# Kernel tuning notes

Hardware: AMD Instinct MI355X
Metric: run time of the kernel (lower is better)

Reference implementation:

```python
import math
import jax, jax.numpy as jnp
import numpy as np

INPUT_DIM = 512
HIDDEN_DIM = 512
BATCH = 8
SEQ_LEN = 4096


def _xavier(key, shape):
    fan_out, fan_in = shape
    limit = math.sqrt(6.0 / (fan_in + fan_out))
    return jax.random.uniform(key, shape, jnp.float32, -limit, limit)


def setup_inputs() -> dict:
    key = jax.random.key(0)
    kx, kA, kB, kC, kD, kWg = jax.random.split(key, 6)
    return {
        "x": jax.random.normal(kx, (BATCH, SEQ_LEN, INPUT_DIM), jnp.float32),
        "A": jax.random.uniform(kA, (HIDDEN_DIM,), jnp.float32, 0.8, 0.95),
        "B": _xavier(kB, (HIDDEN_DIM, INPUT_DIM)),
        "C": _xavier(kC, (HIDDEN_DIM, HIDDEN_DIM)),
        "D": _xavier(kD, (HIDDEN_DIM, INPUT_DIM)),
        "Wg": _xavier(kWg, (HIDDEN_DIM, INPUT_DIM)),
        "bias_h": jnp.zeros((HIDDEN_DIM,), jnp.float32),
        "bias_y": jnp.zeros((HIDDEN_DIM,), jnp.float32),
    }


def reference(x, A, B, C, D, Wg, bias_h, bias_y):
    # x: (b, t, i). Eval mode: dropout is identity.
    hidden_dim = A.shape[0]
    # Precompute all input-dependent per-step terms as batched GEMMs.
    g = jnp.clip(jax.nn.sigmoid(jnp.einsum('bti,hi->bth', x, Wg)), 0.05, 0.95)
    xB = jnp.einsum('bti,hi->bth', x, B)
    # h_t = h_{t-1} + g_t*(A*h_{t-1} + xB_t + bias_h - h_{t-1})
    #     = (1 - g_t*(1 - A)) * h_{t-1} + g_t*(xB_t + bias_h)
    a_coef = 1.0 - g * (1.0 - A)          # (b, t, h)
    b_coef = g * (xB + bias_h)            # (b, t, h)

    def step(h, ab):
        a_t, b_t = ab
        h = a_t * h + b_t
        return h, h

    h0 = jnp.zeros((x.shape[0], hidden_dim), x.dtype)
    _, hs = jax.lax.scan(step, h0, (jnp.swapaxes(a_coef, 0, 1), jnp.swapaxes(b_coef, 0, 1)))
    hs = jnp.swapaxes(hs, 0, 1)           # (b, t, h)

    scale = 1.0 / math.sqrt(hidden_dim)
    y = (jnp.einsum('bth,oh->bto', hs, C) + jnp.einsum('bti,hi->bth', x, D) + bias_y) * scale
    return y
```

## Files before the change

### kernel.cpp

```cpp
#include <hip/hip_runtime.h>
#include <math.h>

#define MTOT 32768
#define KD 512
#define HD 512
#define NB 8
#define TS 4096
#define NCHUNK 64
#define TCHUNK 64

typedef __attribute__((ext_vector_type(8))) short bf16x8;
typedef __attribute__((ext_vector_type(4))) float f32x4;
typedef __attribute__((ext_vector_type(4))) unsigned short us4;

#define GLD16(gsrc, ldst) __builtin_amdgcn_global_load_lds( \
    (const __attribute__((address_space(1))) void*)(gsrc),   \
    (__attribute__((address_space(3))) void*)(ldst), 16, 0, 0)

__device__ __forceinline__ unsigned short f2bf(float f) {
    unsigned u = __float_as_uint(f);
    return (unsigned short)((u + 0x7FFFu + ((u >> 16) & 1u)) >> 16);
}
__device__ __forceinline__ float bf2f(unsigned short u) {
    return __uint_as_float(((unsigned)u) << 16);
}

__global__ __launch_bounds__(256) void cast_all(
    const float* __restrict__ x, const float* __restrict__ B,
    const float* __restrict__ G, const float* __restrict__ C,
    const float* __restrict__ D,
    unsigned short* __restrict__ x16, unsigned short* __restrict__ w16)
{
    const int blk = blockIdx.x;
    const float* src;
    unsigned short* dst;
    int i;
    if (blk < (MTOT * KD / 1024)) {
        src = x; dst = x16;
        i = blk * 1024 + threadIdx.x * 4;
    } else {
        const int r = blk - (MTOT * KD / 1024);
        const int mat = r >> 8;
        src = (mat == 0) ? B : (mat == 1) ? G : (mat == 2) ? C : D;
        dst = w16 + (size_t)mat * (HD * KD);
        i = (r & 255) * 1024 + threadIdx.x * 4;
    }
    float4 v = *(const float4*)(src + i);
    us4 o; o.x = f2bf(v.x); o.y = f2bf(v.y); o.z = f2bf(v.z); o.w = f2bf(v.w);
    *(us4*)(dst + i) = o;
}

__global__ __launch_bounds__(256, 3) void in_gemm_mfma(
    const short* __restrict__ xb, const short* __restrict__ wmat,
    const float* __restrict__ Avec, const float* __restrict__ bias_h,
    unsigned* __restrict__ ab16, float2* __restrict__ chPS)
{
    __shared__ __align__(16) short Xs[128 * 64];
    __shared__ __align__(16) short Ws[2][64 * 64];
    const int tid = threadIdx.x;
    const int w = tid >> 6, l = tid & 63;
    const int m0 = blockIdx.x * 128;
    const int n0 = blockIdx.y * 64;
    const int wm = (w & 1) * 64;
    const int wn = (w >> 1) * 32;

    int xsrc[4], xdst[4];
    #pragma unroll
    for (int j = 0; j < 4; ++j) {
        const int s = (w * 4 + j) * 64 + l;
        const int r = s >> 3, g = (s & 7) ^ (r & 7);
        xsrc[j] = (m0 + r) * KD + g * 8;
        xdst[j] = (w * 4 + j) * 64 * 8;
    }
    int wsrc[2], wdst[2];
    #pragma unroll
    for (int j = 0; j < 2; ++j) {
        const int s = (w * 2 + j) * 64 + l;
        const int r = s >> 3, g = (s & 7) ^ (r & 7);
        wsrc[j] = (n0 + r) * KD + g * 8;
        wdst[j] = (w * 2 + j) * 64 * 8;
    }

    f32x4 acc[2][4][2];
    #pragma unroll
    for (int a = 0; a < 2; ++a)
        #pragma unroll
        for (int i = 0; i < 4; ++i)
            #pragma unroll
            for (int j = 0; j < 2; ++j) acc[a][i][j] = (f32x4)0.0f;

    for (int kk = 0; kk < KD; kk += 64) {
        __syncthreads();
        #pragma unroll
        for (int j = 0; j < 4; ++j) GLD16(xb + xsrc[j] + kk, Xs + xdst[j]);
        #pragma unroll
        for (int mat = 0; mat < 2; ++mat)
            #pragma unroll
            for (int j = 0; j < 2; ++j)
                GLD16(wmat + (size_t)mat * (HD * KD) + wsrc[j] + kk, &Ws[mat][wdst[j]]);
        __syncthreads();
        #pragma unroll
        for (int kc = 0; kc < 2; ++kc) {
            const int g = kc * 4 + (l >> 4);
            bf16x8 af[4];
            #pragma unroll
            for (int mt = 0; mt < 4; ++mt) {
                const int r = wm + mt * 16 + (l & 15);
                af[mt] = *(const bf16x8*)(Xs + r * 64 + ((g ^ (r & 7)) * 8));
            }
            #pragma unroll
            for (int mat = 0; mat < 2; ++mat) {
                #pragma unroll
                for (int nt = 0; nt < 2; ++nt) {
                    const int r = wn + nt * 16 + (l & 15);
                    bf16x8 bfv = *(const bf16x8*)(&Ws[mat][r * 64 + ((g ^ (r & 7)) * 8)]);
                    #pragma unroll
                    for (int mt = 0; mt < 4; ++mt)
                        acc[mat][mt][nt] = __builtin_amdgcn_mfma_f32_16x16x32_bf16(
                            af[mt], bfv, acc[mat][mt][nt], 0, 0, 0);
                }
            }
        }
    }

    const int q  = l >> 4;
    const int cl = l & 15;
    const int bidx   = m0 >> 12;
    const int c_in_b = ((m0 & (TS - 1)) >> 6) + (w & 1);
    #pragma unroll
    for (int nt = 0; nt < 2; ++nt) {
        const int n = n0 + wn + nt * 16 + cl;
        const float An1 = 1.0f - Avec[n];
        const float bh  = bias_h[n];
        float Pc = 1.0f, Sc = 0.0f;
        #pragma unroll
        for (int mt = 0; mt < 4; ++mt) {
            float Pl = 1.0f, Sl = 0.0f;
            #pragma unroll
            for (int r = 0; r < 4; ++r) {
                const float vB = acc[0][mt][nt][r];
                const float vG = acc[1][mt][nt][r];
                float g = __builtin_amdgcn_rcpf(1.0f + __expf(-vG));
                g = fminf(fmaxf(g, 0.05f), 0.95f);
                const unsigned short su = f2bf(g * An1);
                const unsigned short bu = f2bf(g * (vB + bh));
                const float a  = 1.0f - bf2f(su);
                const float bb = bf2f(bu);
                const int m = m0 + wm + mt * 16 + q * 4 + r;
                ab16[(size_t)m * HD + n] = (unsigned)su | ((unsigned)bu << 16);
                Sl = fmaf(a, Sl, bb);
                Pl *= a;
            }
            float Pm = 1.0f, Sm = 0.0f;
            #pragma unroll
            for (int k = 0; k < 4; ++k) {
                const float Pk = __shfl(Pl, cl + 16 * k, 64);
                const float Sk = __shfl(Sl, cl + 16 * k, 64);
                Sm = fmaf(Pk, Sm, Sk);
                Pm *= Pk;
            }
            Sc = fmaf(Pm, Sc, Sm);
            Pc *= Pm;
        }
        if (q == 0) {
            chPS[(size_t)c_in_b * (NB * HD) + bidx * HD + n] = make_float2(Pc, Sc);
        }
    }
}

__global__ __launch_bounds__(256) void scan_pass3(
    const unsigned* __restrict__ ab, const float2* __restrict__ chPS,
    unsigned short* __restrict__ hs_out)
{
    const int g = blockIdx.x * blockDim.x + threadIdx.x;
    const int h = g & (HD - 1);
    const int rest = g >> 9;
    const int b = rest & (NB - 1);
    const int c = rest >> 3;
    const float2* p = chPS + (size_t)b * HD + h;
    float hv = 0.0f;
    for (int j = 0; j < c; ++j) {
        const float2 ps = p[(size_t)j * (NB * HD)];
        hv = fmaf(ps.x, hv, ps.y);
    }
    size_t idx = ((size_t)(b * TS + c * TCHUNK)) * HD + h;
    #pragma unroll 4
    for (int t = 0; t < TCHUNK; ++t) {
        const unsigned v = ab[idx];
        const float a  = 1.0f - bf2f((unsigned short)(v & 0xFFFFu));
        const float bb = bf2f((unsigned short)(v >> 16));
        hv = fmaf(a, hv, bb);
        hs_out[idx] = f2bf(hv);
        idx += HD;
    }
}

__global__ __launch_bounds__(256, 2) void out_gemm_dual(
    const short* __restrict__ hs, const short* __restrict__ xb,
    const short* __restrict__ Cb, const short* __restrict__ Db,
    const float* __restrict__ bias_y, float* __restrict__ y)
{
    __shared__ __align__(16) short Hs[128 * 64];
    __shared__ __align__(16) short Xs2[128 * 64];
    __shared__ __align__(16) short Cs[128 * 64];
    __shared__ __align__(16) short Ds[128 * 64];
    const int tid = threadIdx.x;
    const int w = tid >> 6, l = tid & 63;
    const int m0 = blockIdx.x * 128;
    const int n0 = blockIdx.y * 128;
    const int wm = (w & 1) * 64;
    const int wn = (w >> 1) * 64;

    int src_m[4], src_n[4], dst_s[4];
    #pragma unroll
    for (int j = 0; j < 4; ++j) {
        const int s = (w * 4 + j) * 64 + l;
        const int r = s >> 3, g = (s & 7) ^ (r & 7);
        src_m[j] = (m0 + r) * HD + g * 8;
        src_n[j] = (n0 + r) * HD + g * 8;
        dst_s[j] = (w * 4 + j) * 64 * 8;
    }

    f32x4 acc[4][4];
    #pragma unroll
    for (int i = 0; i < 4; ++i)
        #pragma unroll
        for (int j = 0; j < 4; ++j) acc[i][j] = (f32x4)0.0f;

    for (int kk = 0; kk < HD; kk += 64) {
        __syncthreads();
        #pragma unroll
        for (int j = 0; j < 4; ++j) {
            GLD16(hs + src_m[j] + kk, Hs  + dst_s[j]);
            GLD16(xb + src_m[j] + kk, Xs2 + dst_s[j]);
            GLD16(Cb + src_n[j] + kk, Cs  + dst_s[j]);
            GLD16(Db + src_n[j] + kk, Ds  + dst_s[j]);
        }
        __syncthreads();
        #pragma unroll
        for (int kc = 0; kc < 2; ++kc) {
            const int g = kc * 4 + (l >> 4);
            {
                bf16x8 af[4], bfv[4];
                #pragma unroll
                for (int t = 0; t < 4; ++t) {
                    const int ra = wm + t * 16 + (l & 15);
                    af[t] = *(const bf16x8*)(Hs + ra * 64 + ((g ^ (ra & 7)) * 8));
                    const int rb = wn + t * 16 + (l & 15);
                    bfv[t] = *(const bf16x8*)(Cs + rb * 64 + ((g ^ (rb & 7)) * 8));
                }
                #pragma unroll
                for (int mt = 0; mt < 4; ++mt)
                    #pragma unroll
                    for (int nt = 0; nt < 4; ++nt)
                        acc[mt][nt] = __builtin_amdgcn_mfma_f32_16x16x32_bf16(
                            af[mt], bfv[nt], acc[mt][nt], 0, 0, 0);
            }
            {
                bf16x8 af[4], bfv[4];
                #pragma unroll
                for (int t = 0; t < 4; ++t) {
                    const int ra = wm + t * 16 + (l & 15);
                    af[t] = *(const bf16x8*)(Xs2 + ra * 64 + ((g ^ (ra & 7)) * 8));
                    const int rb = wn + t * 16 + (l & 15);
                    bfv[t] = *(const bf16x8*)(Ds + rb * 64 + ((g ^ (rb & 7)) * 8));
                }
                #pragma unroll
                for (int mt = 0; mt < 4; ++mt)
                    #pragma unroll
                    for (int nt = 0; nt < 4; ++nt)
                        acc[mt][nt] = __builtin_amdgcn_mfma_f32_16x16x32_bf16(
                            af[mt], bfv[nt], acc[mt][nt], 0, 0, 0);
            }
        }
    }

    const float scale = 0.04419417382415922f;
    #pragma unroll
    for (int nt = 0; nt < 4; ++nt) {
        const int n = n0 + wn + nt * 16 + (l & 15);
        const float by = bias_y[n];
        #pragma unroll
        for (int mt = 0; mt < 4; ++mt) {
            #pragma unroll
            for (int r = 0; r < 4; ++r) {
                const int m = m0 + wm + mt * 16 + (l >> 4) * 4 + r;
                y[(size_t)m * HD + n] = (acc[mt][nt][r] + by) * scale;
            }
        }
    }
}

extern "C" void kernel_launch(void* const* d_in, const int* in_sizes, int n_in,
                              void* d_out, int out_size, void* d_ws, size_t ws_size,
                              hipStream_t stream) {
    const float* x      = (const float*)d_in[0];
    const float* Avec   = (const float*)d_in[1];
    const float* Bw     = (const float*)d_in[2];
    const float* Cw     = (const float*)d_in[3];
    const float* Dw     = (const float*)d_in[4];
    const float* Wg     = (const float*)d_in[5];
    const float* bias_h = (const float*)d_in[6];
    const float* bias_y = (const float*)d_in[7];
    float* y = (float*)d_out;

    unsigned* ab16        = (unsigned*)d_ws;
    unsigned short* x16   = (unsigned short*)(ab16 + (size_t)MTOT * HD);
    unsigned short* hs16  = x16 + (size_t)MTOT * HD;
    unsigned short* w16   = hs16 + (size_t)MTOT * HD;
    float2* chPS = (float2*)(w16 + (size_t)4 * HD * KD);

    cast_all<<<MTOT * KD / 1024 + 4 * (HD * KD / 1024), 256, 0, stream>>>(
        x, Bw, Wg, Cw, Dw, x16, w16);

    in_gemm_mfma<<<dim3(MTOT / 128, HD / 64), 256, 0, stream>>>(
        (const short*)x16, (const short*)w16, Avec, bias_h, ab16, chPS);

    scan_pass3<<<(NB * HD * NCHUNK) / 256, 256, 0, stream>>>(ab16, chPS, hs16);

    out_gemm_dual<<<dim3(MTOT / 128, HD / 128), 256, 0, stream>>>(
        (const short*)hs16, (const short*)x16,
        (const short*)(w16 + (size_t)2 * HD * KD),
        (const short*)(w16 + (size_t)3 * HD * KD), bias_y, y);
}
```

Baseline: 248.9 us.

## Fuse chunked scan into input GEMM using decoupled lookback across blocks

Merges the scan pass into the input GEMM kernel. Blocks take a dynamic virtual id from an atomic counter, publish per-tile chunk aggregates with release flags, and walk back over predecessor aggregates to get the carry-in state. Each block then finishes the recurrence in registers and writes bf16 hidden states through an LDS transpose. This drops the packed a/b intermediate (a full global write and read) and one kernel launch. In exchange it adds a serial lookback that grows with position in the sequence, spin-waiting on other blocks, and a bounded guard that could produce wrong results if it ever times out.

```diff
diff --git a/kernel.cpp b/kernel.cpp
--- a/kernel.cpp
+++ b/kernel.cpp
@@ -6,8 +6,6 @@
 #define HD 512
 #define NB 8
 #define TS 4096
-#define NCHUNK 64
-#define TCHUNK 64
 
 typedef __attribute__((ext_vector_type(8))) short bf16x8;
 typedef __attribute__((ext_vector_type(4))) float f32x4;
@@ -29,9 +27,13 @@
     const float* __restrict__ x, const float* __restrict__ B,
     const float* __restrict__ G, const float* __restrict__ C,
     const float* __restrict__ D,
-    unsigned short* __restrict__ x16, unsigned short* __restrict__ w16)
+    unsigned short* __restrict__ x16, unsigned short* __restrict__ w16,
+    unsigned* __restrict__ flags)
 {
     const int blk = blockIdx.x;
+    if (blk == 0) {
+        for (int i = threadIdx.x; i < 2049; i += 256) flags[i] = 0u;
+    }
     const float* src;
     unsigned short* dst;
     int i;
@@ -50,17 +52,35 @@
     *(us4*)(dst + i) = o;
 }
 
-__global__ __launch_bounds__(256, 3) void in_gemm_mfma(
+__global__ __launch_bounds__(256, 3) void in_gemm_scan(
     const short* __restrict__ xb, const short* __restrict__ wmat,
     const float* __restrict__ Avec, const float* __restrict__ bias_h,
-    unsigned* __restrict__ ab16, float2* __restrict__ chPS)
+    unsigned short* __restrict__ hs_out,
+    unsigned long long* __restrict__ payload,
+    unsigned* __restrict__ flags)
 {
-    __shared__ __align__(16) short Xs[128 * 64];
-    __shared__ __align__(16) short Ws[2][64 * 64];
+    __shared__ __align__(16) char smem[(128 * 64 + 2 * 64 * 64) * 2];
+    short* Xs  = (short*)smem;
+    short* Ws0 = Xs + 128 * 64;
+    short* Ws1 = Ws0 + 64 * 64;
+    short* hsT = (short*)smem;
+    __shared__ float2 chunkAgg[2][64];
+    __shared__ float Eblk[64];
+    __shared__ unsigned vid_s;
+
     const int tid = threadIdx.x;
+    if (tid == 0) vid_s = atomicAdd(flags + 2048, 1u);
+    __syncthreads();
+    const unsigned vid = vid_s;
+    const int mxG = vid >> 3;
+    const int ny  = vid & 7;
+    const int m0 = mxG * 128;
+    const int n0 = ny * 64;
+    const int batch = mxG >> 5;
+    const int pos   = mxG & 31;
+    const int base_f = ny * 256 + batch * 32;
+
     const int w = tid >> 6, l = tid & 63;
-    const int m0 = blockIdx.x * 128;
-    const int n0 = blockIdx.y * 64;
     const int wm = (w & 1) * 64;
     const int wn = (w >> 1) * 32;
 
@@ -94,10 +114,10 @@
         #pragma unroll
         for (int j = 0; j < 4; ++j) GLD16(xb + xsrc[j] + kk, Xs + xdst[j]);
         #pragma unroll
-        for (int mat = 0; mat < 2; ++mat)
-            #pragma unroll
-            for (int j = 0; j < 2; ++j)
-                GLD16(wmat + (size_t)mat * (HD * KD) + wsrc[j] + kk, &Ws[mat][wdst[j]]);
+        for (int j = 0; j < 2; ++j) {
+            GLD16(wmat + wsrc[j] + kk, Ws0 + wdst[j]);
+            GLD16(wmat + (size_t)(HD * KD) + wsrc[j] + kk, Ws1 + wdst[j]);
+        }
         __syncthreads();
         #pragma unroll
         for (int kc = 0; kc < 2; ++kc) {
@@ -109,15 +129,17 @@
                 af[mt] = *(const bf16x8*)(Xs + r * 64 + ((g ^ (r & 7)) * 8));
             }
             #pragma unroll
-            for (int mat = 0; mat < 2; ++mat) {
-                #pragma unroll
-                for (int nt = 0; nt < 2; ++nt) {
-                    const int r = wn + nt * 16 + (l & 15);
-                    bf16x8 bfv = *(const bf16x8*)(&Ws[mat][r * 64 + ((g ^ (r & 7)) * 8)]);
-                    #pragma unroll
-                    for (int mt = 0; mt < 4; ++mt)
-                        acc[mat][mt][nt] = __builtin_amdgcn_mfma_f32_16x16x32_bf16(
-                            af[mt], bfv, acc[mat][mt][nt], 0, 0, 0);
+            for (int nt = 0; nt < 2; ++nt) {
+                const int r = wn + nt * 16 + (l & 15);
+                const int off = r * 64 + ((g ^ (r & 7)) * 8);
+                const bf16x8 bfB = *(const bf16x8*)(Ws0 + off);
+                const bf16x8 bfG = *(const bf16x8*)(Ws1 + off);
+                #pragma unroll
+                for (int mt = 0; mt < 4; ++mt) {
+                    acc[0][mt][nt] = __builtin_amdgcn_mfma_f32_16x16x32_bf16(
+                        af[mt], bfB, acc[0][mt][nt], 0, 0, 0);
+                    acc[1][mt][nt] = __builtin_amdgcn_mfma_f32_16x16x32_bf16(
+                        af[mt], bfG, acc[1][mt][nt], 0, 0, 0);
                 }
             }
         }
@@ -125,8 +147,7 @@
 
     const int q  = l >> 4;
     const int cl = l & 15;
-    const int bidx   = m0 >> 12;
-    const int c_in_b = ((m0 & (TS - 1)) >> 6) + (w & 1);
+    unsigned ab_pack[2][16];
     #pragma unroll
     for (int nt = 0; nt < 2; ++nt) {
         const int n = n0 + wn + nt * 16 + cl;
@@ -144,11 +165,9 @@
                 g = fminf(fmaxf(g, 0.05f), 0.95f);
                 const unsigned short su = f2bf(g * An1);
                 const unsigned short bu = f2bf(g * (vB + bh));
-                const float a  = 1.0f - bf2f(su);
-                const float bb = bf2f(bu);
-                const int m = m0 + wm + mt * 16 + q * 4 + r;
-                ab16[(size_t)m * HD + n] = (unsigned)su | ((unsigned)bu << 16);
-                Sl = fmaf(a, Sl, bb);
+                ab_pack[nt][mt * 4 + r] = (unsigned)su | ((unsigned)bu << 16);
+                const float a = 1.0f - bf2f(su);
+                Sl = fmaf(a, Sl, bf2f(bu));
                 Pl *= a;
             }
             float Pm = 1.0f, Sm = 0.0f;
@@ -162,36 +181,87 @@
             Sc = fmaf(Pm, Sc, Sm);
             Pc *= Pm;
         }
-        if (q == 0) {
-            chPS[(size_t)c_in_b * (NB * HD) + bidx * HD + n] = make_float2(Pc, Sc);
-        }
-    }
-}
-
-__global__ __launch_bounds__(256) void scan_pass3(
-    const unsigned* __restrict__ ab, const float2* __restrict__ chPS,
-    unsigned short* __restrict__ hs_out)
-{
-    const int g = blockIdx.x * blockDim.x + threadIdx.x;
-    const int h = g & (HD - 1);
-    const int rest = g >> 9;
-    const int b = rest & (NB - 1);
-    const int c = rest >> 3;
-    const float2* p = chPS + (size_t)b * HD + h;
-    float hv = 0.0f;
-    for (int j = 0; j < c; ++j) {
-        const float2 ps = p[(size_t)j * (NB * HD)];
-        hv = fmaf(ps.x, hv, ps.y);
-    }
-    size_t idx = ((size_t)(b * TS + c * TCHUNK)) * HD + h;
-    #pragma unroll 4
-    for (int t = 0; t < TCHUNK; ++t) {
-        const unsigned v = ab[idx];
-        const float a  = 1.0f - bf2f((unsigned short)(v & 0xFFFFu));
-        const float bb = bf2f((unsigned short)(v >> 16));
-        hv = fmaf(a, hv, bb);
-        hs_out[idx] = f2bf(hv);
-        idx += HD;
+        if (q == 0) chunkAgg[w & 1][wn + nt * 16 + cl] = make_float2(Pc, Sc);
+    }
+    __syncthreads();
+
+    if (tid < 64) {
+        const float2 c0 = chunkAgg[0][tid], c1 = chunkAgg[1][tid];
+        union { float2 f; unsigned long long u; } cv;
+        cv.f = make_float2(c1.x * c0.x, fmaf(c1.x, c0.y, c1.y));
+        __hip_atomic_store(&payload[(size_t)(base_f + pos) * 64 + tid], cv.u,
+                           __ATOMIC_RELAXED, __HIP_MEMORY_SCOPE_AGENT);
+    }
+    __syncthreads();
+    if (tid == 0)
+        __hip_atomic_store(&flags[base_f + pos], 1u,
+                           __ATOMIC_RELEASE, __HIP_MEMORY_SCOPE_AGENT);
+
+    if (tid < 64) {
+        float Pa = 1.0f, Sa = 0.0f;
+        for (int p = pos - 1; p >= 0; --p) {
+            int guard = 0;
+            while (__hip_atomic_load(&flags[base_f + p], __ATOMIC_ACQUIRE,
+                                     __HIP_MEMORY_SCOPE_AGENT) == 0u) {
+                __builtin_amdgcn_s_sleep(8);
+                if (++guard > (1 << 22)) break;
+            }
+            union { float2 f; unsigned long long u; } cv;
+            cv.u = __hip_atomic_load(&payload[(size_t)(base_f + p) * 64 + tid],
+                                     __ATOMIC_RELAXED, __HIP_MEMORY_SCOPE_AGENT);
+            Sa = fmaf(Pa, cv.f.y, Sa);
+            Pa *= cv.f.x;
+        }
+        Eblk[tid] = Sa;
+    }
+    __syncthreads();
+
+    #pragma unroll
+    for (int nt = 0; nt < 2; ++nt) {
+        const int hcol = wn + nt * 16 + cl;
+        float E_run = Eblk[hcol];
+        if (w & 1) {
+            const float2 c0 = chunkAgg[0][hcol];
+            E_run = fmaf(c0.x, E_run, c0.y);
+        }
+        #pragma unroll
+        for (int mt = 0; mt < 4; ++mt) {
+            float av[4], bv[4];
+            float Pl = 1.0f, Sl = 0.0f;
+            #pragma unroll
+            for (int r = 0; r < 4; ++r) {
+                const unsigned pk = ab_pack[nt][mt * 4 + r];
+                av[r] = 1.0f - bf2f((unsigned short)(pk & 0xFFFFu));
+                bv[r] = bf2f((unsigned short)(pk >> 16));
+                Sl = fmaf(av[r], Sl, bv[r]);
+                Pl *= av[r];
+            }
+            float Pacc = 1.0f, Sacc = 0.0f, Pq = 1.0f, Sq = 0.0f;
+            #pragma unroll
+            for (int k = 0; k < 4; ++k) {
+                const float Pk = __shfl(Pl, cl + 16 * k, 64);
+                const float Sk = __shfl(Sl, cl + 16 * k, 64);
+                if (k == q) { Pq = Pacc; Sq = Sacc; }
+                Sacc = fmaf(Pk, Sacc, Sk);
+                Pacc *= Pk;
+            }
+            float hv = fmaf(Pq, E_run, Sq);
+            #pragma unroll
+            for (int r = 0; r < 4; ++r) {
+                hv = fmaf(av[r], hv, bv[r]);
+                hsT[(wm + mt * 16 + q * 4 + r) * 72 + hcol] = (short)f2bf(hv);
+            }
+            E_run = fmaf(Pacc, E_run, Sacc);
+        }
+    }
+    __syncthreads();
+
+    #pragma unroll
+    for (int it = 0; it < 4; ++it) {
+        const int o = it * 2048 + tid * 8;
+        const int row = o >> 6, col = o & 63;
+        const bf16x8 v = *(const bf16x8*)(hsT + row * 72 + col);
+        *(bf16x8*)(hs_out + (size_t)(m0 + row) * HD + n0 + col) = v;
     }
 }
 
@@ -304,19 +374,17 @@
     const float* bias_y = (const float*)d_in[7];
     float* y = (float*)d_out;
 
-    unsigned* ab16        = (unsigned*)d_ws;
-    unsigned short* x16   = (unsigned short*)(ab16 + (size_t)MTOT * HD);
-    unsigned short* hs16  = x16 + (size_t)MTOT * HD;
-    unsigned short* w16   = hs16 + (size_t)MTOT * HD;
-    float2* chPS = (float2*)(w16 + (size_t)4 * HD * KD);
+    unsigned short* x16  = (unsigned short*)d_ws;
+    unsigned short* hs16 = x16 + (size_t)MTOT * KD;
+    unsigned short* w16  = hs16 + (size_t)MTOT * HD;
+    unsigned long long* payload = (unsigned long long*)(w16 + (size_t)4 * HD * KD);
+    unsigned* flags = (unsigned*)(payload + (size_t)2048 * 64);
 
     cast_all<<<MTOT * KD / 1024 + 4 * (HD * KD / 1024), 256, 0, stream>>>(
-        x, Bw, Wg, Cw, Dw, x16, w16);
-
-    in_gemm_mfma<<<dim3(MTOT / 128, HD / 64), 256, 0, stream>>>(
-        (const short*)x16, (const short*)w16, Avec, bias_h, ab16, chPS);
-
-    scan_pass3<<<(NB * HD * NCHUNK) / 256, 256, 0, stream>>>(ab16, chPS, hs16);
+        x, Bw, Wg, Cw, Dw, x16, w16, flags);
+
+    in_gemm_scan<<<2048, 256, 0, stream>>>(
+        (const short*)x16, (const short*)w16, Avec, bias_h, hs16, payload, flags);
 
     out_gemm_dual<<<dim3(MTOT / 128, HD / 128), 256, 0, stream>>>(
         (const short*)hs16, (const short*)x16,
```

Result: slower. 532.3 us (+113.8%).
